# Optimization experiments

Hardware: AMD Instinct MI355X
Metric: run time of the kernel (lower is better)

Reference implementation:

```python
import jax, jax.numpy as jnp
import numpy as np

D_MODEL = 1024
N_HEADS = 16
HEAD_DIM = D_MODEL // N_HEADS
ROPE_BASE = 10000.0
B, S = 2, 2048


def _rope_cos_sin(seq_len):
    inv_freq = 1.0 / (ROPE_BASE ** (jnp.arange(0, HEAD_DIM, 2, dtype=jnp.float32) / HEAD_DIM))
    t = jnp.arange(seq_len, dtype=jnp.float32)
    freqs = jnp.outer(t, inv_freq)                 # [S, HEAD_DIM/2]
    emb = jnp.concatenate([freqs, freqs], axis=-1)  # [S, HEAD_DIM]
    return jnp.cos(emb), jnp.sin(emb)


def _apply_rope(x, cos, sin):
    # x: [B, H, S, D]; cos/sin: [S, D]
    x1 = x[..., ::2]
    x2 = x[..., 1::2]
    return jnp.concatenate(
        [x1 * cos[..., ::2] - x2 * sin[..., ::2],
         x1 * sin[..., 1::2] + x2 * cos[..., 1::2]], axis=-1)


def setup_inputs() -> dict:
    key = jax.random.key(0)
    ks = jax.random.split(key, 5)
    std = 1.0 / np.sqrt(D_MODEL)
    x = jax.random.normal(ks[0], (B, S, D_MODEL), dtype=jnp.float32)
    Wq = jax.random.normal(ks[1], (D_MODEL, D_MODEL), dtype=jnp.float32) * std
    Wk = jax.random.normal(ks[2], (D_MODEL, D_MODEL), dtype=jnp.float32) * std
    Wv = jax.random.normal(ks[3], (D_MODEL, D_MODEL), dtype=jnp.float32) * std
    Wo = jax.random.normal(ks[4], (D_MODEL, D_MODEL), dtype=jnp.float32) * std
    attn_mask = jnp.tril(jnp.ones((S, S), dtype=jnp.int32))  # 0 = masked (causal)
    return {"x": x, "Wq": Wq, "Wk": Wk, "Wv": Wv, "Wo": Wo, "attn_mask": attn_mask}


def reference(x, Wq, Wk, Wv, Wo, attn_mask):
    b, s, _ = x.shape
    scale = 1.0 / np.sqrt(HEAD_DIM)
    # torch Linear: y = x @ W.T
    q = (x @ Wq.T).reshape(b, s, N_HEADS, HEAD_DIM).transpose(0, 2, 1, 3)
    k = (x @ Wk.T).reshape(b, s, N_HEADS, HEAD_DIM).transpose(0, 2, 1, 3)
    v = (x @ Wv.T).reshape(b, s, N_HEADS, HEAD_DIM).transpose(0, 2, 1, 3)
    cos, sin = _rope_cos_sin(s)
    q = _apply_rope(q, cos, sin)
    k = _apply_rope(k, cos, sin)
    scores = jnp.einsum('bhqd,bhkd->bhqk', q, k) * scale  # [B,H,S,S]
    scores = jnp.where(attn_mask == 0, -jnp.inf, scores)
    attn = jax.nn.softmax(scores, axis=-1)
    out = jnp.einsum('bhqk,bhkd->bhqd', attn, v)
    out = out.transpose(0, 2, 1, 3).reshape(b, s, D_MODEL)
    return out @ Wo.T
```

## Files before the change

kernel.cpp:

```cpp
#include <hip/hip_runtime.h>
#include <hip/hip_bf16.h>
#include <cstdint>

#define SEQ 2048
#define NH  16
#define HD  64
#define DM  1024
#define BATCH 2

typedef unsigned short ushort_t;
typedef __attribute__((ext_vector_type(8))) short short8;
typedef __attribute__((ext_vector_type(4))) float f32x4;

__device__ __forceinline__ ushort_t f2bf(float f){
  __hip_bfloat16 h = __float2bfloat16(f);
  return *reinterpret_cast<ushort_t*>(&h);
}
__device__ __forceinline__ ushort_t f2bf_fast(float f){
  uint32_t u = __float_as_uint(f);
  u += 0x7FFF + ((u >> 16) & 1);
  return (ushort_t)(u >> 16);
}

#define GLDS(g, l) __builtin_amdgcn_global_load_lds( \
    (const __attribute__((address_space(1))) void*)(g), \
    (__attribute__((address_space(3))) void*)(l), 16, 0, 0)

__device__ __forceinline__ void rope_tab_elem(float* __restrict__ tab, int idx){
  int t = idx & 2047, j = idx >> 11;
  float invf = exp2f(-(float)j * 0.41524101186092033f);
  float sn, cn;
  sincosf((float)t * invf, &sn, &cn);
  tab[2*idx]   = cn;
  tab[2*idx+1] = sn;
}

__global__ __launch_bounds__(256) void rope_tab_kernel(float* __restrict__ tab){
  rope_tab_elem(tab, blockIdx.x * 256 + threadIdx.x);
}

__global__ __launch_bounds__(256) void prep_kernel(
    const float* __restrict__ x,  const float* __restrict__ Wq,
    const float* __restrict__ Wk, const float* __restrict__ Wv,
    const float* __restrict__ Wo,
    ushort_t* __restrict__ xb,  ushort_t* __restrict__ wqb,
    ushort_t* __restrict__ wkb, ushort_t* __restrict__ wvb,
    ushort_t* __restrict__ wob, float* __restrict__ tab)
{
  int bid = blockIdx.x;
  if(bid >= 8192){
    rope_tab_elem(tab, (bid - 8192) * 256 + threadIdx.x);
    return;
  }
  int f = bid * 256 + threadIdx.x;
  const float* s; ushort_t* d; int off;
  if(f < (1<<20)){ s = x; d = xb; off = f; }
  else{
    int r = f - (1<<20);
    int w = r >> 18;
    off = r & ((1<<18)-1);
    s = (w==0)?Wq:(w==1)?Wk:(w==2)?Wv:Wo;
    d = (w==0)?wqb:(w==1)?wkb:(w==2)?wvb:wob;
  }
  float4 v = *reinterpret_cast<const float4*>(s + (size_t)off*4);
  ushort_t t[4] = {f2bf(v.x), f2bf(v.y), f2bf(v.z), f2bf(v.w)};
  *reinterpret_cast<uint2*>(d + (size_t)off*4) = *reinterpret_cast<const uint2*>(t);
}

template<bool SWAP>
__device__ __forceinline__ void gemm_core_bf16_glds(
    const ushort_t* __restrict__ A, const ushort_t* __restrict__ B,
    ushort_t* As, ushort_t* Bs,
    int m0, int n0, f32x4 acc[4][4])
{
  const int tid  = threadIdx.x;
  const int lane = tid & 63;
  const int wave = tid >> 6;
  const int quad = lane >> 4, l16 = lane & 15;
  const int wm = (wave >> 1) * 64, wn = (wave & 1) * 64;

  const int srow0 = tid >> 2, sseg0 = tid & 3;

  #define STAGE_BF16(k0, hb) { \
    _Pragma("unroll") \
    for(int u = 0; u < 2; u++){ \
      int idx = tid + u * 256; \
      int row = srow0 + u * 64, seg = sseg0; \
      int col = (seg ^ (row & 3)) * 8; \
      ushort_t* la = &As[(hb)*4096 + (size_t)(idx & ~63) * 8]; \
      ushort_t* lb = &Bs[(hb)*4096 + (size_t)(idx & ~63) * 8]; \
      GLDS(&A[(size_t)(m0+row)*DM + (k0) + col], la); \
      GLDS(&B[(size_t)(n0+row)*DM + (k0) + col], lb); \
    } }

  STAGE_BF16(0, 0);
  __syncthreads();
  int cur = 0;
  for(int k0 = 0; k0 < DM; k0 += 32){
    if(k0 + 32 < DM) STAGE_BF16(k0 + 32, cur ^ 1);
    const ushort_t* as = &As[cur*4096];
    const ushort_t* bs = &Bs[cur*4096];
    short8 af[4], bf[4];
    #pragma unroll
    for(int mt=0;mt<4;mt++){
      int row = wm + mt*16 + l16;
      af[mt] = *reinterpret_cast<const short8*>(&as[row*32 + (quad ^ (row&3))*8]);
    }
    #pragma unroll
    for(int nt=0;nt<4;nt++){
      int row = wn + nt*16 + l16;
      bf[nt] = *reinterpret_cast<const short8*>(&bs[row*32 + (quad ^ (row&3))*8]);
    }
    #pragma unroll
    for(int mt=0;mt<4;mt++)
      #pragma unroll
      for(int nt=0;nt<4;nt++)
        acc[mt][nt] = SWAP
          ? __builtin_amdgcn_mfma_f32_16x16x32_bf16(bf[nt], af[mt], acc[mt][nt], 0, 0, 0)
          : __builtin_amdgcn_mfma_f32_16x16x32_bf16(af[mt], bf[nt], acc[mt][nt], 0, 0, 0);
    __syncthreads();
    cur ^= 1;
  }
  #undef STAGE_BF16
}

template<bool SWAP>
__device__ __forceinline__ void gemm_core_f32(
    const float* __restrict__ A, const float* __restrict__ B,
    ushort_t* As, ushort_t* Bs, int m0, int n0, f32x4 acc[4][4])
{
  const int tid  = threadIdx.x;
  const int lane = tid & 63;
  const int wave = tid >> 6;
  const int quad = lane >> 4, l16 = lane & 15;
  const int wm = (wave >> 1) * 64, wn = (wave & 1) * 64;
  for(int k0 = 0; k0 < DM; k0 += 32){
    #pragma unroll
    for(int u = 0; u < 4; u++){
      int idx = tid + u * 256;
      int row = idx >> 3, seg = idx & 7;
      float4 av = *reinterpret_cast<const float4*>(&A[(size_t)(m0+row)*DM + k0 + seg*4]);
      float4 bv = *reinterpret_cast<const float4*>(&B[(size_t)(n0+row)*DM + k0 + seg*4]);
      ushort_t at[4] = {f2bf(av.x), f2bf(av.y), f2bf(av.z), f2bf(av.w)};
      ushort_t bt[4] = {f2bf(bv.x), f2bf(bv.y), f2bf(bv.z), f2bf(bv.w)};
      *reinterpret_cast<uint2*>(&As[row*40 + seg*4]) = *reinterpret_cast<const uint2*>(at);
      *reinterpret_cast<uint2*>(&Bs[row*40 + seg*4]) = *reinterpret_cast<const uint2*>(bt);
    }
    __syncthreads();
    short8 af[4], bf[4];
    #pragma unroll
    for(int mt=0;mt<4;mt++) af[mt] = *reinterpret_cast<const short8*>(&As[(wm+mt*16+l16)*40 + quad*8]);
    #pragma unroll
    for(int nt=0;nt<4;nt++) bf[nt] = *reinterpret_cast<const short8*>(&Bs[(wn+nt*16+l16)*40 + quad*8]);
    #pragma unroll
    for(int mt=0;mt<4;mt++)
      #pragma unroll
      for(int nt=0;nt<4;nt++)
        acc[mt][nt] = SWAP
          ? __builtin_amdgcn_mfma_f32_16x16x32_bf16(bf[nt], af[mt], acc[mt][nt], 0, 0, 0)
          : __builtin_amdgcn_mfma_f32_16x16x32_bf16(af[mt], bf[nt], acc[mt][nt], 0, 0, 0);
    __syncthreads();
  }
}

__device__ __forceinline__ void qkv_epilogue_swap(
    int z, int m0, int n0, f32x4 acc[4][4], const float* __restrict__ tab,
    ushort_t* __restrict__ Q, ushort_t* __restrict__ Ko, ushort_t* __restrict__ Vt)
{
  const int lane = threadIdx.x & 63;
  const int wave = threadIdx.x >> 6;
  const int quad = lane >> 4, l16 = lane & 15;
  const int wm = (wave >> 1) * 64, wn = (wave & 1) * 64;
  if(z < 2){
    ushort_t* outp = (z == 0) ? Q : Ko;
    const float qscale = (z == 0) ? 0.125f : 1.0f;
    #pragma unroll
    for(int mt=0;mt<4;mt++){
      int m = m0 + wm + mt*16 + l16;
      int b = m >> 11, s = m & 2047;
      #pragma unroll
      for(int nt=0;nt<4;nt++){
        int nbase = n0 + wn + nt*16 + quad*4;
        int h  = nbase >> 6, dhb = nbase & 63;
        int jb = dhb & 31;
        float v0 = acc[mt][nt][0], v1 = acc[mt][nt][1];
        float v2 = acc[mt][nt][2], v3 = acc[mt][nt][3];
        float2 cs0 = *reinterpret_cast<const float2*>(&tab[((jb  )*SEQ + s)*2]);
        float2 cs1 = *reinterpret_cast<const float2*>(&tab[((jb+1)*SEQ + s)*2]);
        float2 cs2 = *reinterpret_cast<const float2*>(&tab[((jb+2)*SEQ + s)*2]);
        float2 cs3 = *reinterpret_cast<const float2*>(&tab[((jb+3)*SEQ + s)*2]);
        float oe0 = (v0*cs0.x - v1*cs0.y) * qscale;
        float oo0 = (v0*cs1.y + v1*cs1.x) * qscale;
        float oe1 = (v2*cs2.x - v3*cs2.y) * qscale;
        float oo1 = (v2*cs3.y + v3*cs3.x) * qscale;
        int d2 = dhb >> 1;
        size_t base = ((size_t)(b*NH + h)*SEQ + s)*HD;
        uint32_t lo = (uint32_t)f2bf_fast(oe0) | ((uint32_t)f2bf_fast(oe1) << 16);
        uint32_t hi = (uint32_t)f2bf_fast(oo0) | ((uint32_t)f2bf_fast(oo1) << 16);
        *reinterpret_cast<uint32_t*>(&outp[base + d2])      = lo;
        *reinterpret_cast<uint32_t*>(&outp[base + d2 + 32]) = hi;
      }
    }
  } else {
    #pragma unroll
    for(int nt=0;nt<4;nt++){
      #pragma unroll
      for(int mt=0;mt<4;mt++){
        int m = m0 + wm + mt*16 + l16;
        int b = m >> 11, s = m & 2047;
        #pragma unroll
        for(int r=0;r<4;r++){
          int n = n0 + wn + nt*16 + quad*4 + r;
          int h = n >> 6, dh = n & 63;
          Vt[((size_t)(b*NH + h)*HD + dh)*SEQ + s] = f2bf_fast(acc[mt][nt][r]);
        }
      }
    }
  }
}

__global__ __launch_bounds__(256) void qkv_bf16_kernel(
    const ushort_t* __restrict__ xb,
    const ushort_t* __restrict__ wqb, const ushort_t* __restrict__ wkb,
    const ushort_t* __restrict__ wvb, const float* __restrict__ tab,
    ushort_t* __restrict__ Q, ushort_t* __restrict__ Ko, ushort_t* __restrict__ Vt)
{
  const int z = blockIdx.z;
  const ushort_t* W = (z == 0) ? wqb : (z == 1) ? wkb : wvb;
  const int m0 = blockIdx.x * 128, n0 = blockIdx.y * 128;
  __shared__ __align__(16) ushort_t As[2*128*32];
  __shared__ __align__(16) ushort_t Bs[2*128*32];
  f32x4 acc[4][4];
  #pragma unroll
  for(int i=0;i<4;i++)
    #pragma unroll
    for(int j=0;j<4;j++) acc[i][j] = (f32x4){0.f,0.f,0.f,0.f};
  gemm_core_bf16_glds<true>(xb, W, As, Bs, m0, n0, acc);
  qkv_epilogue_swap(z, m0, n0, acc, tab, Q, Ko, Vt);
}

__global__ __launch_bounds__(256) void qkv_f32_kernel(
    const float* __restrict__ x,
    const float* __restrict__ Wq, const float* __restrict__ Wk,
    const float* __restrict__ Wv, const float* __restrict__ tab,
    ushort_t* __restrict__ Q, ushort_t* __restrict__ Ko, ushort_t* __restrict__ Vt)
{
  const int z = blockIdx.z;
  const float* W = (z == 0) ? Wq : (z == 1) ? Wk : Wv;
  const int m0 = blockIdx.x * 128, n0 = blockIdx.y * 128;
  __shared__ __align__(16) char smem[20480];
  ushort_t* As = (ushort_t*)smem;
  ushort_t* Bs = (ushort_t*)(smem + 10240);
  f32x4 acc[4][4];
  #pragma unroll
  for(int i=0;i<4;i++)
    #pragma unroll
    for(int j=0;j<4;j++) acc[i][j] = (f32x4){0.f,0.f,0.f,0.f};
  gemm_core_f32<true>(x, W, As, Bs, m0, n0, acc);
  qkv_epilogue_swap(z, m0, n0, acc, tab, Q, Ko, Vt);
}

__global__ __launch_bounds__(256) void attn_kernel(
    ushort_t* __restrict__ Qbuf, const ushort_t* __restrict__ K,
    const ushort_t* __restrict__ Vt)
{
  const int bh = blockIdx.x;
  const int y  = blockIdx.y;
  const int g  = (y < 8) ? (15 - y) : (y - 8);
  const int T  = 2*(g+1);
  const int tid  = threadIdx.x;
  const int lane = tid & 63;
  const int wave = tid >> 6;
  const int quad = lane >> 4, l16 = lane & 15;

  ushort_t*       Qp = Qbuf + (size_t)bh * SEQ * HD;
  const ushort_t* Kp = K    + (size_t)bh * SEQ * HD;
  const ushort_t* Vp = Vt   + (size_t)bh * HD * SEQ;

  __shared__ __align__(16) ushort_t Ks[64*72];
  __shared__ __align__(16) ushort_t Vs[64*72];
  __shared__ __align__(16) ushort_t Pl[4][32*72];
  ushort_t* pl = &Pl[wave][0];

  const int srow0 = tid >> 3;
  const int scol  = (tid & 7) * 8;

  const int q0w = 128*g + 32*wave;

  short8 qf[2][2];
  #pragma unroll
  for(int s=0;s<2;s++)
    #pragma unroll
    for(int kk=0;kk<2;kk++)
      qf[s][kk] = *reinterpret_cast<const short8*>(&Qp[(size_t)(q0w + 16*s + l16)*HD + kk*32 + quad*8]);

  f32x4 oacc[2][4];
  #pragma unroll
  for(int s=0;s<2;s++)
    #pragma unroll
    for(int dt=0;dt<4;dt++) oacc[s][dt] = (f32x4){0.f,0.f,0.f,0.f};
  float llane[2] = {0.f, 0.f};

  uint4 kreg[2], vreg[2];
  #pragma unroll
  for(int u=0;u<2;u++){
    int row = srow0 + u*32;
    kreg[u] = *reinterpret_cast<const uint4*>(&Kp[(size_t)row*HD + scol]);
    vreg[u] = *reinterpret_cast<const uint4*>(&Vp[(size_t)row*SEQ + scol]);
  }

  for(int t = 0; t < T; t++){
    const int kv0 = t * 64;

    __syncthreads();
    #pragma unroll
    for(int u=0;u<2;u++){
      int row = srow0 + u*32;
      *reinterpret_cast<uint4*>(&Ks[row*72 + scol]) = kreg[u];
      *reinterpret_cast<uint4*>(&Vs[row*72 + scol]) = vreg[u];
    }
    __syncthreads();

    if(t < T-1){
      #pragma unroll
      for(int u=0;u<2;u++){
        int row = srow0 + u*32;
        kreg[u] = *reinterpret_cast<const uint4*>(&Kp[(size_t)(kv0 + 64 + row)*HD + scol]);
        vreg[u] = *reinterpret_cast<const uint4*>(&Vp[(size_t)row*SEQ + kv0 + 64 + scol]);
      }
    }

    short8 kf[4][2], vf[4][2];
    #pragma unroll
    for(int nt=0;nt<4;nt++)
      #pragma unroll
      for(int kk=0;kk<2;kk++)
        kf[nt][kk] = *reinterpret_cast<const short8*>(&Ks[(nt*16 + l16)*72 + kk*32 + quad*8]);
    #pragma unroll
    for(int dt=0;dt<4;dt++)
      #pragma unroll
      for(int kk=0;kk<2;kk++)
        vf[dt][kk] = *reinterpret_cast<const short8*>(&Vs[(dt*16 + l16)*72 + kk*32 + quad*8]);

    #pragma unroll
    for(int s=0;s<2;s++){
      f32x4 sacc[4];
      #pragma unroll
      for(int nt=0;nt<4;nt++) sacc[nt] = (f32x4){0.f,0.f,0.f,0.f};
      #pragma unroll
      for(int kk=0;kk<2;kk++)
        #pragma unroll
        for(int nt=0;nt<4;nt++)
          sacc[nt] = __builtin_amdgcn_mfma_f32_16x16x32_bf16(kf[nt][kk], qf[s][kk], sacc[nt], 0,0,0);

      const int q_abs = q0w + 16*s + l16;
      const bool maskable = (kv0 + 63 > q0w + 16*s);
      float pv[4][4];
      #pragma unroll
      for(int nt=0;nt<4;nt++)
        #pragma unroll
        for(int r=0;r<4;r++){
          float sv = sacc[nt][r];
          if(maskable){
            int kv_abs = kv0 + nt*16 + quad*4 + r;
            sv = (kv_abs > q_abs) ? -1e30f : sv;
          }
          float p = __expf(sv);
          pv[nt][r] = p;
          llane[s] += p;
        }

      asm volatile("" ::: "memory");
      #pragma unroll
      for(int nt=0;nt<4;nt++){
        uint32_t lo = (uint32_t)f2bf_fast(pv[nt][0]) | ((uint32_t)f2bf_fast(pv[nt][1]) << 16);
        uint32_t hi = (uint32_t)f2bf_fast(pv[nt][2]) | ((uint32_t)f2bf_fast(pv[nt][3]) << 16);
        uint2 pk; pk.x = lo; pk.y = hi;
        *reinterpret_cast<uint2*>(&pl[(16*s + l16)*72 + nt*16 + quad*4]) = pk;
      }
      asm volatile("s_waitcnt lgkmcnt(0)" ::: "memory");

      #pragma unroll
      for(int kk=0;kk<2;kk++){
        short8 pf = *reinterpret_cast<const short8*>(&pl[(16*s + l16)*72 + kk*32 + quad*8]);
        #pragma unroll
        for(int dt=0;dt<4;dt++)
          oacc[s][dt] = __builtin_amdgcn_mfma_f32_16x16x32_bf16(vf[dt][kk], pf, oacc[s][dt], 0,0,0);
      }
    }
  }

  #pragma unroll
  for(int s=0;s<2;s++){
    float lt = llane[s];
    lt += __shfl_xor(lt, 16);
    lt += __shfl_xor(lt, 32);
    float inv = 1.0f / lt;
    #pragma unroll
    for(int dt=0;dt<4;dt++){
      uint32_t lo = (uint32_t)f2bf_fast(oacc[s][dt][0] * inv) | ((uint32_t)f2bf_fast(oacc[s][dt][1] * inv) << 16);
      uint32_t hi = (uint32_t)f2bf_fast(oacc[s][dt][2] * inv) | ((uint32_t)f2bf_fast(oacc[s][dt][3] * inv) << 16);
      uint2 pk; pk.x = lo; pk.y = hi;
      *reinterpret_cast<uint2*>(&Qp[(size_t)(q0w + 16*s + l16)*HD + dt*16 + quad*4]) = pk;
    }
  }
}

__global__ __launch_bounds__(256) void out_proj_bf16_kernel(
    const ushort_t* __restrict__ ctx, const ushort_t* __restrict__ wob,
    float* __restrict__ out)
{
  const int m0 = blockIdx.x * 128, n0 = blockIdx.y * 128;
  __shared__ __align__(16) ushort_t As[2*128*32];
  __shared__ __align__(16) ushort_t Bs[2*128*32];
  const int tid  = threadIdx.x;
  const int lane = tid & 63;
  const int wave = tid >> 6;
  const int quad = lane >> 4, l16 = lane & 15;
  const int wm = (wave >> 1) * 64, wn = (wave & 1) * 64;
  const int srow0 = tid >> 2, sseg0 = tid & 3;

  f32x4 acc[4][4];
  #pragma unroll
  for(int i=0;i<4;i++)
    #pragma unroll
    for(int j=0;j<4;j++) acc[i][j] = (f32x4){0.f,0.f,0.f,0.f};

  #define STAGE_OP(k0, hb) { \
    const int head = (k0) >> 6, off = (k0) & 63; \
    _Pragma("unroll") \
    for(int u = 0; u < 2; u++){ \
      int idx = tid + u * 256; \
      int row = srow0 + u * 64, seg = sseg0; \
      int col = (seg ^ (row & 3)) * 8; \
      int m = m0 + row, b = m >> 11, s = m & 2047; \
      ushort_t* la = &As[(hb)*4096 + (size_t)(idx & ~63) * 8]; \
      ushort_t* lb = &Bs[(hb)*4096 + (size_t)(idx & ~63) * 8]; \
      GLDS(&ctx[((size_t)(b*NH + head)*SEQ + s)*HD + off + col], la); \
      GLDS(&wob[(size_t)(n0+row)*DM + (k0) + col], lb); \
    } }

  STAGE_OP(0, 0);
  __syncthreads();
  int cur = 0;
  for(int k0 = 0; k0 < DM; k0 += 32){
    if(k0 + 32 < DM) STAGE_OP(k0 + 32, cur ^ 1);
    const ushort_t* as = &As[cur*4096];
    const ushort_t* bs = &Bs[cur*4096];
    short8 af[4], bf[4];
    #pragma unroll
    for(int mt=0;mt<4;mt++){
      int row = wm + mt*16 + l16;
      af[mt] = *reinterpret_cast<const short8*>(&as[row*32 + (quad ^ (row&3))*8]);
    }
    #pragma unroll
    for(int nt=0;nt<4;nt++){
      int row = wn + nt*16 + l16;
      bf[nt] = *reinterpret_cast<const short8*>(&bs[row*32 + (quad ^ (row&3))*8]);
    }
    #pragma unroll
    for(int mt=0;mt<4;mt++)
      #pragma unroll
      for(int nt=0;nt<4;nt++)
        acc[mt][nt] = __builtin_amdgcn_mfma_f32_16x16x32_bf16(af[mt], bf[nt], acc[mt][nt], 0, 0, 0);
    __syncthreads();
    cur ^= 1;
  }
  #undef STAGE_OP

  #pragma unroll
  for(int mt=0;mt<4;mt++)
    #pragma unroll
    for(int nt=0;nt<4;nt++)
      #pragma unroll
      for(int r=0;r<4;r++){
        int m = m0 + wm + mt*16 + quad*4 + r;
        int n = n0 + wn + nt*16 + l16;
        out[(size_t)m*DM + n] = acc[mt][nt][r];
      }
}

__global__ __launch_bounds__(256) void out_proj_f32_kernel(
    const ushort_t* __restrict__ ctx, const float* __restrict__ Wo,
    float* __restrict__ out)
{
  const int m0 = blockIdx.x * 128, n0 = blockIdx.y * 128;
  __shared__ __align__(16) ushort_t As[128*40];
  __shared__ __align__(16) ushort_t Bs[128*40];
  const int tid  = threadIdx.x;
  const int lane = tid & 63;
  const int wave = tid >> 6;
  const int quad = lane >> 4, l16 = lane & 15;
  const int wm = (wave >> 1) * 64, wn = (wave & 1) * 64;

  f32x4 acc[4][4];
  #pragma unroll
  for(int i=0;i<4;i++)
    #pragma unroll
    for(int j=0;j<4;j++) acc[i][j] = (f32x4){0.f,0.f,0.f,0.f};

  for(int k0 = 0; k0 < DM; k0 += 32){
    const int head = k0 >> 6, off = k0 & 63;
    #pragma unroll
    for(int u = 0; u < 2; u++){
      int idx = tid + u * 256;
      int row = idx >> 2, seg = idx & 3;
      int m = m0 + row, b = m >> 11, s = m & 2047;
      *reinterpret_cast<uint4*>(&As[row*40 + seg*8]) =
        *reinterpret_cast<const uint4*>(&ctx[((size_t)(b*NH + head)*SEQ + s)*HD + off + seg*8]);
    }
    #pragma unroll
    for(int u = 0; u < 4; u++){
      int idx = tid + u * 256;
      int row = idx >> 3, seg = idx & 7;
      float4 bv = *reinterpret_cast<const float4*>(&Wo[(size_t)(n0+row)*DM + k0 + seg*4]);
      ushort_t bt[4] = {f2bf(bv.x), f2bf(bv.y), f2bf(bv.z), f2bf(bv.w)};
      *reinterpret_cast<uint2*>(&Bs[row*40 + seg*4]) = *reinterpret_cast<const uint2*>(bt);
    }
    __syncthreads();
    short8 af[4], bf[4];
    #pragma unroll
    for(int mt=0;mt<4;mt++) af[mt] = *reinterpret_cast<const short8*>(&As[(wm+mt*16+l16)*40 + quad*8]);
    #pragma unroll
    for(int nt=0;nt<4;nt++) bf[nt] = *reinterpret_cast<const short8*>(&Bs[(wn+nt*16+l16)*40 + quad*8]);
    #pragma unroll
    for(int mt=0;mt<4;mt++)
      #pragma unroll
      for(int nt=0;nt<4;nt++)
        acc[mt][nt] = __builtin_amdgcn_mfma_f32_16x16x32_bf16(af[mt], bf[nt], acc[mt][nt], 0, 0, 0);
    __syncthreads();
  }
  #pragma unroll
  for(int mt=0;mt<4;mt++)
    #pragma unroll
    for(int nt=0;nt<4;nt++)
      #pragma unroll
      for(int r=0;r<4;r++){
        int m = m0 + wm + mt*16 + quad*4 + r;
        int n = n0 + wn + nt*16 + l16;
        out[(size_t)m*DM + n] = acc[mt][nt][r];
      }
}

extern "C" void kernel_launch(void* const* d_in, const int* in_sizes, int n_in,
                              void* d_out, int out_size, void* d_ws, size_t ws_size,
                              hipStream_t stream) {
  const float* x  = (const float*)d_in[0];
  const float* Wq = (const float*)d_in[1];
  const float* Wk = (const float*)d_in[2];
  const float* Wv = (const float*)d_in[3];
  const float* Wo = (const float*)d_in[4];
  float* out = (float*)d_out;

  char* ws = (char*)d_ws;
  ushort_t* Qb  = (ushort_t*)ws;
  float*    tab = (float*)(ws + (8u << 20));
  ushort_t* Kb  = (ushort_t*)d_out;
  ushort_t* Vt  = (ushort_t*)d_out + (size_t)BATCH*NH*SEQ*HD;

  const bool big_ws = ws_size >= (25u << 20);

  if(big_ws){
    ushort_t* xb  = (ushort_t*)(ws + (8u  << 20) + (512u << 10));
    char*     wb0 = ws + (16u << 20) + (512u << 10);
    ushort_t* wqb = (ushort_t*)(wb0);
    ushort_t* wkb = (ushort_t*)(wb0 + (2u << 20));
    ushort_t* wvb = (ushort_t*)(wb0 + (4u << 20));
    ushort_t* wob = (ushort_t*)(wb0 + (6u << 20));
    prep_kernel<<<8448, 256, 0, stream>>>(x, Wq, Wk, Wv, Wo, xb, wqb, wkb, wvb, wob, tab);
    dim3 g1(32, 8, 3);
    qkv_bf16_kernel<<<g1, 256, 0, stream>>>(xb, wqb, wkb, wvb, tab, Qb, Kb, Vt);
    dim3 g2(32, 16);
    attn_kernel<<<g2, 256, 0, stream>>>(Qb, Kb, Vt);
    dim3 g3(32, 8);
    out_proj_bf16_kernel<<<g3, 256, 0, stream>>>(Qb, wob, out);
  } else {
    rope_tab_kernel<<<256, 256, 0, stream>>>(tab);
    dim3 g1(32, 8, 3);
    qkv_f32_kernel<<<g1, 256, 0, stream>>>(x, Wq, Wk, Wv, tab, Qb, Kb, Vt);
    dim3 g2(32, 16);
    attn_kernel<<<g2, 256, 0, stream>>>(Qb, Kb, Vt);
    dim3 g3(32, 8);
    out_proj_f32_kernel<<<g3, 256, 0, stream>>>(Qb, Wo, out);
  }
}
```

Measured before the change: 238.4 us.

## Double-buffer K/V shared tiles to cut one barrier per iteration

The attention kernel now keeps two shared-memory buffers for the K and V tiles. Each iteration writes the next tile into the spare buffer while computing on the current one, and prefetches global data two tiles ahead. This drops from two __syncthreads per iteration to one and overlaps LDS stores with compute. The cost is doubled K/V shared memory, which may lower occupancy, plus longer register lifetimes for the prefetch.

```diff
diff --git a/kernel.cpp b/kernel.cpp
--- a/kernel.cpp
+++ b/kernel.cpp
@@ -277,8 +277,8 @@
   const ushort_t* Kp = K    + (size_t)bh * SEQ * HD;
   const ushort_t* Vp = Vt   + (size_t)bh * HD * SEQ;
 
-  __shared__ __align__(16) ushort_t Ks[64*72];
-  __shared__ __align__(16) ushort_t Vs[64*72];
+  __shared__ __align__(16) ushort_t Ks[2][64*72];
+  __shared__ __align__(16) ushort_t Vs[2][64*72];
   __shared__ __align__(16) ushort_t Pl[4][32*72];
   ushort_t* pl = &Pl[wave][0];
 
@@ -308,39 +308,54 @@
     kreg[u] = *reinterpret_cast<const uint4*>(&Kp[(size_t)row*HD + scol]);
     vreg[u] = *reinterpret_cast<const uint4*>(&Vp[(size_t)row*SEQ + scol]);
   }
+  #pragma unroll
+  for(int u=0;u<2;u++){
+    int row = srow0 + u*32;
+    *reinterpret_cast<uint4*>(&Ks[0][row*72 + scol]) = kreg[u];
+    *reinterpret_cast<uint4*>(&Vs[0][row*72 + scol]) = vreg[u];
+  }
+  if(T > 1){
+    #pragma unroll
+    for(int u=0;u<2;u++){
+      int row = srow0 + u*32;
+      kreg[u] = *reinterpret_cast<const uint4*>(&Kp[(size_t)(64 + row)*HD + scol]);
+      vreg[u] = *reinterpret_cast<const uint4*>(&Vp[(size_t)row*SEQ + 64 + scol]);
+    }
+  }
+  __syncthreads();
 
   for(int t = 0; t < T; t++){
     const int kv0 = t * 64;
-
-    __syncthreads();
-    #pragma unroll
-    for(int u=0;u<2;u++){
-      int row = srow0 + u*32;
-      *reinterpret_cast<uint4*>(&Ks[row*72 + scol]) = kreg[u];
-      *reinterpret_cast<uint4*>(&Vs[row*72 + scol]) = vreg[u];
-    }
-    __syncthreads();
-
-    if(t < T-1){
+    const int cur = t & 1;
+
+    short8 kf[4][2], vf[4][2];
+    #pragma unroll
+    for(int nt=0;nt<4;nt++)
+      #pragma unroll
+      for(int kk=0;kk<2;kk++)
+        kf[nt][kk] = *reinterpret_cast<const short8*>(&Ks[cur][(nt*16 + l16)*72 + kk*32 + quad*8]);
+    #pragma unroll
+    for(int dt=0;dt<4;dt++)
+      #pragma unroll
+      for(int kk=0;kk<2;kk++)
+        vf[dt][kk] = *reinterpret_cast<const short8*>(&Vs[cur][(dt*16 + l16)*72 + kk*32 + quad*8]);
+
+    if(t + 1 < T){
       #pragma unroll
       for(int u=0;u<2;u++){
         int row = srow0 + u*32;
-        kreg[u] = *reinterpret_cast<const uint4*>(&Kp[(size_t)(kv0 + 64 + row)*HD + scol]);
-        vreg[u] = *reinterpret_cast<const uint4*>(&Vp[(size_t)row*SEQ + kv0 + 64 + scol]);
-      }
-    }
-
-    short8 kf[4][2], vf[4][2];
-    #pragma unroll
-    for(int nt=0;nt<4;nt++)
-      #pragma unroll
-      for(int kk=0;kk<2;kk++)
-        kf[nt][kk] = *reinterpret_cast<const short8*>(&Ks[(nt*16 + l16)*72 + kk*32 + quad*8]);
-    #pragma unroll
-    for(int dt=0;dt<4;dt++)
-      #pragma unroll
-      for(int kk=0;kk<2;kk++)
-        vf[dt][kk] = *reinterpret_cast<const short8*>(&Vs[(dt*16 + l16)*72 + kk*32 + quad*8]);
+        *reinterpret_cast<uint4*>(&Ks[cur^1][row*72 + scol]) = kreg[u];
+        *reinterpret_cast<uint4*>(&Vs[cur^1][row*72 + scol]) = vreg[u];
+      }
+    }
+    if(t + 2 < T){
+      #pragma unroll
+      for(int u=0;u<2;u++){
+        int row = srow0 + u*32;
+        kreg[u] = *reinterpret_cast<const uint4*>(&Kp[(size_t)(kv0 + 128 + row)*HD + scol]);
+        vreg[u] = *reinterpret_cast<const uint4*>(&Vp[(size_t)row*SEQ + kv0 + 128 + scol]);
+      }
+    }
 
     #pragma unroll
     for(int s=0;s<2;s++){
@@ -388,6 +403,7 @@
           oacc[s][dt] = __builtin_amdgcn_mfma_f32_16x16x32_bf16(vf[dt][kk], pf, oacc[s][dt], 0,0,0);
       }
     }
+    __syncthreads();
   }
 
   #pragma unroll
```

Result: no change. 236.8 us, median of 4 (-0.7%).

## Halve attention query tile per block to 64 rows and double grid

Applied to the files above, without the earlier changes.

Each attention block now handles 64 query rows (16 per wave) instead of 128, and the grid doubles to 32x32 blocks. A new four-group mapping of blockIdx.y interleaves long and short causal tiles to balance load. V fragments are loaded from LDS inside the PV loop instead of being preloaded, which cuts register pressure. The trade-off is that K/V tiles are now loaded and staged through LDS twice as often across blocks for the same query range.

```diff
diff --git a/kernel.cpp b/kernel.cpp
--- a/kernel.cpp
+++ b/kernel.cpp
@@ -264,10 +264,11 @@
     ushort_t* __restrict__ Qbuf, const ushort_t* __restrict__ K,
     const ushort_t* __restrict__ Vt)
 {
-  const int bh = blockIdx.x;
-  const int y  = blockIdx.y;
-  const int g  = (y < 8) ? (15 - y) : (y - 8);
-  const int T  = 2*(g+1);
+  const int bh  = blockIdx.x;
+  const int yy  = blockIdx.y;
+  const int grp = yy >> 3, yi = yy & 7;
+  const int qb  = (grp==0) ? 31-yi : (grp==1) ? yi : (grp==2) ? 23-yi : 8+yi;
+  const int T   = qb + 1;
   const int tid  = threadIdx.x;
   const int lane = tid & 63;
   const int wave = tid >> 6;
@@ -279,27 +280,23 @@
 
   __shared__ __align__(16) ushort_t Ks[64*72];
   __shared__ __align__(16) ushort_t Vs[64*72];
-  __shared__ __align__(16) ushort_t Pl[4][32*72];
+  __shared__ __align__(16) ushort_t Pl[4][16*72];
   ushort_t* pl = &Pl[wave][0];
 
   const int srow0 = tid >> 3;
   const int scol  = (tid & 7) * 8;
 
-  const int q0w = 128*g + 32*wave;
-
-  short8 qf[2][2];
-  #pragma unroll
-  for(int s=0;s<2;s++)
-    #pragma unroll
-    for(int kk=0;kk<2;kk++)
-      qf[s][kk] = *reinterpret_cast<const short8*>(&Qp[(size_t)(q0w + 16*s + l16)*HD + kk*32 + quad*8]);
-
-  f32x4 oacc[2][4];
-  #pragma unroll
-  for(int s=0;s<2;s++)
-    #pragma unroll
-    for(int dt=0;dt<4;dt++) oacc[s][dt] = (f32x4){0.f,0.f,0.f,0.f};
-  float llane[2] = {0.f, 0.f};
+  const int q0w = 64*qb + 32*0 + 16*wave;
+
+  short8 qf[2];
+  #pragma unroll
+  for(int kk=0;kk<2;kk++)
+    qf[kk] = *reinterpret_cast<const short8*>(&Qp[(size_t)(q0w + l16)*HD + kk*32 + quad*8]);
+
+  f32x4 oacc[4];
+  #pragma unroll
+  for(int dt=0;dt<4;dt++) oacc[dt] = (f32x4){0.f,0.f,0.f,0.f};
+  float llane = 0.f;
 
   uint4 kreg[2], vreg[2];
   #pragma unroll
@@ -330,79 +327,69 @@
       }
     }
 
-    short8 kf[4][2], vf[4][2];
+    short8 kf[4][2];
     #pragma unroll
     for(int nt=0;nt<4;nt++)
       #pragma unroll
       for(int kk=0;kk<2;kk++)
         kf[nt][kk] = *reinterpret_cast<const short8*>(&Ks[(nt*16 + l16)*72 + kk*32 + quad*8]);
-    #pragma unroll
-    for(int dt=0;dt<4;dt++)
-      #pragma unroll
-      for(int kk=0;kk<2;kk++)
-        vf[dt][kk] = *reinterpret_cast<const short8*>(&Vs[(dt*16 + l16)*72 + kk*32 + quad*8]);
-
-    #pragma unroll
-    for(int s=0;s<2;s++){
-      f32x4 sacc[4];
-      #pragma unroll
-      for(int nt=0;nt<4;nt++) sacc[nt] = (f32x4){0.f,0.f,0.f,0.f};
-      #pragma unroll
-      for(int kk=0;kk<2;kk++)
-        #pragma unroll
-        for(int nt=0;nt<4;nt++)
-          sacc[nt] = __builtin_amdgcn_mfma_f32_16x16x32_bf16(kf[nt][kk], qf[s][kk], sacc[nt], 0,0,0);
-
-      const int q_abs = q0w + 16*s + l16;
-      const bool maskable = (kv0 + 63 > q0w + 16*s);
-      float pv[4][4];
+
+    f32x4 sacc[4];
+    #pragma unroll
+    for(int nt=0;nt<4;nt++) sacc[nt] = (f32x4){0.f,0.f,0.f,0.f};
+    #pragma unroll
+    for(int kk=0;kk<2;kk++)
       #pragma unroll
       for(int nt=0;nt<4;nt++)
-        #pragma unroll
-        for(int r=0;r<4;r++){
-          float sv = sacc[nt][r];
-          if(maskable){
-            int kv_abs = kv0 + nt*16 + quad*4 + r;
-            sv = (kv_abs > q_abs) ? -1e30f : sv;
-          }
-          float p = __expf(sv);
-          pv[nt][r] = p;
-          llane[s] += p;
+        sacc[nt] = __builtin_amdgcn_mfma_f32_16x16x32_bf16(kf[nt][kk], qf[kk], sacc[nt], 0,0,0);
+
+    const int q_abs = q0w + l16;
+    const bool maskable = (kv0 + 63 > q0w);
+    #pragma unroll
+    for(int nt=0;nt<4;nt++)
+      #pragma unroll
+      for(int r=0;r<4;r++){
+        float sv = sacc[nt][r];
+        if(maskable){
+          int kv_abs = kv0 + nt*16 + quad*4 + r;
+          sv = (kv_abs > q_abs) ? -1e30f : sv;
         }
-
-      asm volatile("" ::: "memory");
-      #pragma unroll
-      for(int nt=0;nt<4;nt++){
-        uint32_t lo = (uint32_t)f2bf_fast(pv[nt][0]) | ((uint32_t)f2bf_fast(pv[nt][1]) << 16);
-        uint32_t hi = (uint32_t)f2bf_fast(pv[nt][2]) | ((uint32_t)f2bf_fast(pv[nt][3]) << 16);
-        uint2 pk; pk.x = lo; pk.y = hi;
-        *reinterpret_cast<uint2*>(&pl[(16*s + l16)*72 + nt*16 + quad*4]) = pk;
-      }
-      asm volatile("s_waitcnt lgkmcnt(0)" ::: "memory");
-
-      #pragma unroll
-      for(int kk=0;kk<2;kk++){
-        short8 pf = *reinterpret_cast<const short8*>(&pl[(16*s + l16)*72 + kk*32 + quad*8]);
-        #pragma unroll
-        for(int dt=0;dt<4;dt++)
-          oacc[s][dt] = __builtin_amdgcn_mfma_f32_16x16x32_bf16(vf[dt][kk], pf, oacc[s][dt], 0,0,0);
-      }
-    }
-  }
-
-  #pragma unroll
-  for(int s=0;s<2;s++){
-    float lt = llane[s];
-    lt += __shfl_xor(lt, 16);
-    lt += __shfl_xor(lt, 32);
-    float inv = 1.0f / lt;
-    #pragma unroll
-    for(int dt=0;dt<4;dt++){
-      uint32_t lo = (uint32_t)f2bf_fast(oacc[s][dt][0] * inv) | ((uint32_t)f2bf_fast(oacc[s][dt][1] * inv) << 16);
-      uint32_t hi = (uint32_t)f2bf_fast(oacc[s][dt][2] * inv) | ((uint32_t)f2bf_fast(oacc[s][dt][3] * inv) << 16);
+        float p = __expf(sv);
+        sacc[nt][r] = p;
+        llane += p;
+      }
+
+    asm volatile("" ::: "memory");
+    #pragma unroll
+    for(int nt=0;nt<4;nt++){
+      uint32_t lo = (uint32_t)f2bf_fast(sacc[nt][0]) | ((uint32_t)f2bf_fast(sacc[nt][1]) << 16);
+      uint32_t hi = (uint32_t)f2bf_fast(sacc[nt][2]) | ((uint32_t)f2bf_fast(sacc[nt][3]) << 16);
       uint2 pk; pk.x = lo; pk.y = hi;
-      *reinterpret_cast<uint2*>(&Qp[(size_t)(q0w + 16*s + l16)*HD + dt*16 + quad*4]) = pk;
-    }
+      *reinterpret_cast<uint2*>(&pl[l16*72 + nt*16 + quad*4]) = pk;
+    }
+    asm volatile("s_waitcnt lgkmcnt(0)" ::: "memory");
+
+    #pragma unroll
+    for(int kk=0;kk<2;kk++){
+      short8 pf = *reinterpret_cast<const short8*>(&pl[l16*72 + kk*32 + quad*8]);
+      #pragma unroll
+      for(int dt=0;dt<4;dt++){
+        short8 vf = *reinterpret_cast<const short8*>(&Vs[(dt*16 + l16)*72 + kk*32 + quad*8]);
+        oacc[dt] = __builtin_amdgcn_mfma_f32_16x16x32_bf16(vf, pf, oacc[dt], 0,0,0);
+      }
+    }
+  }
+
+  float lt = llane;
+  lt += __shfl_xor(lt, 16);
+  lt += __shfl_xor(lt, 32);
+  float inv = 1.0f / lt;
+  #pragma unroll
+  for(int dt=0;dt<4;dt++){
+    uint32_t lo = (uint32_t)f2bf_fast(oacc[dt][0] * inv) | ((uint32_t)f2bf_fast(oacc[dt][1] * inv) << 16);
+    uint32_t hi = (uint32_t)f2bf_fast(oacc[dt][2] * inv) | ((uint32_t)f2bf_fast(oacc[dt][3] * inv) << 16);
+    uint2 pk; pk.x = lo; pk.y = hi;
+    *reinterpret_cast<uint2*>(&Qp[(size_t)(q0w + l16)*HD + dt*16 + quad*4]) = pk;
   }
 }
 
@@ -570,7 +557,7 @@
     prep_kernel<<<8448, 256, 0, stream>>>(x, Wq, Wk, Wv, Wo, xb, wqb, wkb, wvb, wob, tab);
     dim3 g1(32, 8, 3);
     qkv_bf16_kernel<<<g1, 256, 0, stream>>>(xb, wqb, wkb, wvb, tab, Qb, Kb, Vt);
-    dim3 g2(32, 16);
+    dim3 g2(32, 32);
     attn_kernel<<<g2, 256, 0, stream>>>(Qb, Kb, Vt);
     dim3 g3(32, 8);
     out_proj_bf16_kernel<<<g3, 256, 0, stream>>>(Qb, wob, out);
@@ -578,7 +565,7 @@
     rope_tab_kernel<<<256, 256, 0, stream>>>(tab);
     dim3 g1(32, 8, 3);
     qkv_f32_kernel<<<g1, 256, 0, stream>>>(x, Wq, Wk, Wv, tab, Qb, Kb, Vt);
-    dim3 g2(32, 16);
+    dim3 g2(32, 32);
     attn_kernel<<<g2, 256, 0, stream>>>(Qb, Kb, Vt);
     dim3 g3(32, 8);
     out_proj_f32_kernel<<<g3, 256, 0, stream>>>(Qb, Wo, out);
```

Measured after the change: 245.6 us. +3.0%, slower.
